# Kernel optimization log

Measured on AMD Instinct MI355X. Metric: run time of the kernel, lower is better.

Reference implementation:

```python
import jax, jax.numpy as jnp
import numpy as np

B, F, E, A = 8192, 50, 16, 16

def setup_inputs() -> dict:
    key = jax.random.key(0)
    ks = jax.random.split(key, 9)
    feat_index = jax.random.randint(ks[0], (B, F), 0, F, dtype=jnp.int64)
    feat_value = jax.random.uniform(ks[1], (B, F), dtype=jnp.float32)
    emb_table = jax.random.uniform(ks[2], (F, E), minval=-0.05, maxval=0.05, dtype=jnp.float32)
    attention_w = 0.05 * jax.random.normal(ks[3], (E, A), dtype=jnp.float32)
    attention_b = 0.05 * jax.random.normal(ks[4], (A,), dtype=jnp.float32)
    attention_h = 0.05 * jax.random.normal(ks[5], (A,), dtype=jnp.float32)
    attention_p = jnp.ones((E, 1), dtype=jnp.float32)
    lin_w = 0.05 * jax.random.normal(ks[6], (F, 1), dtype=jnp.float32)
    lin_b = jnp.zeros((1,), dtype=jnp.float32)
    return {"feat_index": feat_index, "feat_value": feat_value, "emb_table": emb_table,
            "attention_w": attention_w, "attention_b": attention_b, "attention_h": attention_h,
            "attention_p": attention_p, "lin_w": lin_w, "lin_b": lin_b}

def reference(feat_index, feat_value, emb_table, attention_w, attention_b, attention_h, attention_p, lin_w, lin_b):
    # embedding lookup + value scaling: [B, F, E]
    emb = emb_table[feat_index] * feat_value[:, :, None]
    # all pairwise (i<j) elementwise products: [B, P, E], P = F*(F-1)/2
    ii, jj = np.triu_indices(emb.shape[1], k=1)
    ewp = emb[:, ii, :] * emb[:, jj, :]
    # attention MLP: relu(ewp @ W + b) . h  -> unnormalized exp scores
    wx = jnp.einsum('bpe,ea->bpa', ewp, attention_w) + attention_b
    score = jnp.exp(jnp.sum(jax.nn.relu(wx) * attention_h, axis=2))  # [B, P]
    att = score / jnp.sum(score, axis=1, keepdims=True)
    # attention-weighted pooling over interactions, then project to scalar
    pooled = jnp.einsum('bp,bpe->be', att, ewp)  # [B, E]
    y_deep = pooled @ attention_p  # [B, 1]
    # linear part: Dense(1, relu) over field axis of emb^T [B, E, F], then sum over E
    y_lin = jnp.sum(jax.nn.relu(jnp.einsum('bfe,fo->beo', emb, lin_w) + lin_b), axis=1)  # [B, 1]
    return y_deep + y_lin
```

## Files before the change

kernel.cpp:

```cpp
#include <hip/hip_runtime.h>
#include <math.h>

#define FDIM  50
#define EDIM  16
#define ADIM  16
#define NPAIR 1225
#define BROWS 32
#define NTHREADS 1024
#define NWAVE 16
#define NPAD  (NPAIR + 2 * NWAVE)
#define FBLK  1024

typedef _Float16 half8v __attribute__((ext_vector_type(8)));
typedef __fp16   h16x8  __attribute__((ext_vector_type(8)));
typedef __fp16   h16x2  __attribute__((ext_vector_type(2)));
typedef float    f32x16 __attribute__((ext_vector_type(16)));

__device__ inline f32x16 mfma32x32x16f16(half8v a, half8v b, f32x16 c) {
    return __builtin_amdgcn_mfma_f32_32x32x16_f16(
        __builtin_bit_cast(h16x8, a), __builtin_bit_cast(h16x8, b), c, 0, 0, 0);
}

__global__ __launch_bounds__(NTHREADS) void afm_fwd(
    const int*   __restrict__ feat_index,
    const float* __restrict__ feat_value,
    const float* __restrict__ emb_table,
    const float* __restrict__ attn_w,
    const float* __restrict__ attn_b,
    const float* __restrict__ attn_h,
    const float* __restrict__ attn_p,
    const float* __restrict__ lin_w,
    const float* __restrict__ lin_b,
    float*       __restrict__ out)
{
    __shared__ __align__(16) _Float16 embLds[FDIM * 512];
    __shared__ unsigned ijLds[NPAD];
    __shared__ float    redLds[NWAVE][BROWS][2];
    __shared__ float    ylinLds[BROWS];
    __shared__ float    lwLds[FDIM];

    const int t    = threadIdx.x;
    const int lane = t & 63;
    const int wv   = t >> 6;
    const int hi   = lane >> 5;
    const int col  = lane & 31;
    const int b0   = blockIdx.x * BROWS;

    if (t < FDIM) lwLds[t] = lin_w[t];

    for (int p = t; p < NPAD; p += NTHREADS) {
        int pc = (p < NPAIR) ? p : NPAIR - 1;
        float tq = 9801.0f - 8.0f * (float)pc;
        int ii = (int)((99.0f - sqrtf(tq)) * 0.5f);
        ii = max(0, min(48, ii));
        while (ii < 48 && (49*(ii+1) - (((ii+1)*ii)>>1)) <= pc) ++ii;
        while (ii > 0  && (49*ii - ((ii*(ii-1))>>1)) > pc) --ii;
        int q  = 49*ii - ((ii*(ii-1))>>1);
        int jj = ii + 1 + (pc - q);
        ijLds[p] = ((unsigned)(ii*FBLK) << 16) | (unsigned)(jj*FBLK);
    }

    for (int f = t >> 6; f < FDIM; f += NWAVE) {
        int   fi = feat_index[(b0 + col) * FDIM + f];
        float fv = feat_value[(b0 + col) * FDIM + f];
        const float4* tr = (const float4*)(emb_table + (size_t)fi * EDIM + hi * 8);
        float4 v0 = tr[0], v1 = tr[1];
        half8v hh;
        hh[0] = (_Float16)(v0.x * fv); hh[1] = (_Float16)(v0.y * fv);
        hh[2] = (_Float16)(v0.z * fv); hh[3] = (_Float16)(v0.w * fv);
        hh[4] = (_Float16)(v1.x * fv); hh[5] = (_Float16)(v1.y * fv);
        hh[6] = (_Float16)(v1.z * fv); hh[7] = (_Float16)(v1.w * fv);
        *(half8v*)&embLds[f * 512 + lane * 8] = hh;
    }
    __syncthreads();

    if (t < 512) {
        int bb = t >> 4, e = t & 15;
        int off = (e >> 3) * 256 + bb * 8 + (e & 7);
        float acc = lin_b[0];
        #pragma unroll
        for (int f = 0; f < FDIM; ++f)
            acc = fmaf((float)embLds[f * 512 + off], lwLds[f], acc);
        acc = fmaxf(acc, 0.0f);
        acc += __shfl_xor(acc, 1);
        acc += __shfl_xor(acc, 2);
        acc += __shfl_xor(acc, 4);
        acc += __shfl_xor(acc, 8);
        if (e == 0) ylinLds[bb] = acc;
    }

    half8v fragA1;
    #pragma unroll
    for (int e = 0; e < 8; ++e) {
        int k = hi * 8 + e;
        float av = (col < ADIM) ? attn_w[k * ADIM + col]
                 : (col == ADIM) ? attn_p[k] : 0.0f;
        fragA1[e] = (_Float16)av;
    }
    half8v fragA2;
    f32x16 biasC;
    #pragma unroll
    for (int e = 0; e < 8; ++e) {
        int r = (e & 3) + 8 * (e >> 2) + 4 * hi;
        fragA2[e]  = (_Float16)(attn_h[r] * 1.44269504f);
        biasC[e]   = attn_b[r];
        biasC[e+8] = 0.f;
    }
    f32x16 zeroC;
    #pragma unroll
    for (int r = 0; r < 16; ++r) zeroC[r] = 0.f;

    const char* ebase = (const char*)embLds;
    const unsigned laddr = (unsigned)lane * 16u;

    float num = 0.f, den = 0.f;
    unsigned u0   = ijLds[wv];
    half8v   ei   = *(const half8v*)(ebase + (u0 >> 16)     + laddr);
    half8v   ej   = *(const half8v*)(ebase + (u0 & 0xffffu) + laddr);
    unsigned unxt = ijLds[wv + NWAVE];

    #pragma unroll 2
    for (int p = wv; p < NPAIR; p += NWAVE) {
        half8v ei_n = *(const half8v*)(ebase + (unxt >> 16)     + laddr);
        half8v ej_n = *(const half8v*)(ebase + (unxt & 0xffffu) + laddr);
        unsigned u2 = ijLds[p + 2 * NWAVE];

        half8v prod = ei * ej;
        f32x16 acc1 = mfma32x32x16f16(fragA1, prod, biasC);

        h16x2 q01 = __builtin_amdgcn_cvt_pkrtz(acc1[0], acc1[1]);
        h16x2 q23 = __builtin_amdgcn_cvt_pkrtz(acc1[2], acc1[3]);
        h16x2 q45 = __builtin_amdgcn_cvt_pkrtz(acc1[4], acc1[5]);
        h16x2 q67 = __builtin_amdgcn_cvt_pkrtz(acc1[6], acc1[7]);
        h16x8 pk = __builtin_shufflevector(
                       __builtin_shufflevector(q01, q23, 0, 1, 2, 3),
                       __builtin_shufflevector(q45, q67, 0, 1, 2, 3),
                       0, 1, 2, 3, 4, 5, 6, 7);
        half8v rf = __builtin_bit_cast(half8v, pk);
        half8v zf;
        #pragma unroll
        for (int e = 0; e < 8; ++e) zf[e] = (_Float16)0;
#if __has_builtin(__builtin_elementwise_max)
        rf = __builtin_elementwise_max(rf, zf);
#else
        #pragma unroll
        for (int e = 0; e < 8; ++e) rf[e] = rf[e] > (_Float16)0 ? rf[e] : (_Float16)0;
#endif
        f32x16 acc2 = mfma32x32x16f16(fragA2, rf, zeroC);

        float sc = __builtin_amdgcn_exp2f(acc2[0]);
        if (hi) den += sc;
        else    num = fmaf(sc, acc1[8], num);

        ei = ei_n; ej = ej_n; unxt = u2;
    }

    if (hi) redLds[wv][col][1] = den;
    else    redLds[wv][col][0] = num;
    __syncthreads();

    if (t < BROWS) {
        float nn = 0.f, dd = 0.f;
        #pragma unroll
        for (int w = 0; w < NWAVE; ++w) { nn += redLds[w][t][0]; dd += redLds[w][t][1]; }
        out[b0 + t] = nn / dd + ylinLds[t];
    }
}

extern "C" void kernel_launch(void* const* d_in, const int* in_sizes, int n_in,
                              void* d_out, int out_size, void* d_ws, size_t ws_size,
                              hipStream_t stream) {
    const int*   feat_index = (const int*)  d_in[0];
    const float* feat_value = (const float*)d_in[1];
    const float* emb_table  = (const float*)d_in[2];
    const float* attn_w     = (const float*)d_in[3];
    const float* attn_b     = (const float*)d_in[4];
    const float* attn_h     = (const float*)d_in[5];
    const float* attn_p     = (const float*)d_in[6];
    const float* lin_w      = (const float*)d_in[7];
    const float* lin_b      = (const float*)d_in[8];
    float* outp = (float*)d_out;

    dim3 grid(out_size / BROWS);
    dim3 block(NTHREADS);
    afm_fwd<<<grid, block, 0, stream>>>(feat_index, feat_value, emb_table,
                                        attn_w, attn_b, attn_h, attn_p,
                                        lin_w, lin_b, outp);
}
```

Measured before the change: 29.83 us.

## Give each wave a contiguous pair chunk and iterate i/j directly

Removes the precomputed pair-index table in LDS. Each wave now takes a contiguous chunk of 77 pairs, finds its starting (i,j) once, and walks j inside nested loops while keeping e_i in registers. This cuts the index loads and the e_i reload per pair. In exchange it adds an inner loop with a variable trip count, which may hurt unrolling, and a prefetch that reads one row past the end (the reason for the padded LDS buffer).

```diff
diff --git a/kernel.cpp b/kernel.cpp
--- a/kernel.cpp
+++ b/kernel.cpp
@@ -8,7 +8,7 @@
 #define BROWS 32
 #define NTHREADS 1024
 #define NWAVE 16
-#define NPAD  (NPAIR + 2 * NWAVE)
+#define CHUNK 77
 #define FBLK  1024
 
 typedef _Float16 half8v __attribute__((ext_vector_type(8)));
@@ -33,11 +33,10 @@
     const float* __restrict__ lin_b,
     float*       __restrict__ out)
 {
-    __shared__ __align__(16) _Float16 embLds[FDIM * 512];
-    __shared__ unsigned ijLds[NPAD];
-    __shared__ float    redLds[NWAVE][BROWS][2];
-    __shared__ float    ylinLds[BROWS];
-    __shared__ float    lwLds[FDIM];
+    __shared__ __align__(16) _Float16 embLds[(FDIM + 1) * 512];
+    __shared__ float redLds[NWAVE][BROWS][2];
+    __shared__ float ylinLds[BROWS];
+    __shared__ float lwLds[FDIM];
 
     const int t    = threadIdx.x;
     const int lane = t & 63;
@@ -47,18 +46,6 @@
     const int b0   = blockIdx.x * BROWS;
 
     if (t < FDIM) lwLds[t] = lin_w[t];
-
-    for (int p = t; p < NPAD; p += NTHREADS) {
-        int pc = (p < NPAIR) ? p : NPAIR - 1;
-        float tq = 9801.0f - 8.0f * (float)pc;
-        int ii = (int)((99.0f - sqrtf(tq)) * 0.5f);
-        ii = max(0, min(48, ii));
-        while (ii < 48 && (49*(ii+1) - (((ii+1)*ii)>>1)) <= pc) ++ii;
-        while (ii > 0  && (49*ii - ((ii*(ii-1))>>1)) > pc) --ii;
-        int q  = 49*ii - ((ii*(ii-1))>>1);
-        int jj = ii + 1 + (pc - q);
-        ijLds[p] = ((unsigned)(ii*FBLK) << 16) | (unsigned)(jj*FBLK);
-    }
 
     for (int f = t >> 6; f < FDIM; f += NWAVE) {
         int   fi = feat_index[(b0 + col) * FDIM + f];
@@ -113,46 +100,59 @@
     const char* ebase = (const char*)embLds;
     const unsigned laddr = (unsigned)lane * 16u;
 
+    const int pbeg = wv * CHUNK;
+    const int pend = (pbeg + CHUNK < NPAIR) ? pbeg + CHUNK : NPAIR;
+
+    float tq = 9801.0f - 8.0f * (float)pbeg;
+    int i = (int)((99.0f - sqrtf(tq)) * 0.5f);
+    i = max(0, min(48, i));
+    while (i < 48 && (49*(i+1) - (((i+1)*i)>>1)) <= pbeg) ++i;
+    while (i > 0  && (49*i - ((i*(i-1))>>1)) > pbeg) --i;
+    int j = i + 1 + (pbeg - (49*i - ((i*(i-1))>>1)));
+
     float num = 0.f, den = 0.f;
-    unsigned u0   = ijLds[wv];
-    half8v   ei   = *(const half8v*)(ebase + (u0 >> 16)     + laddr);
-    half8v   ej   = *(const half8v*)(ebase + (u0 & 0xffffu) + laddr);
-    unsigned unxt = ijLds[wv + NWAVE];
+    int p = pbeg;
+    while (p < pend) {
+        int len = FDIM - j;
+        if (len > pend - p) len = pend - p;
+        half8v ei = *(const half8v*)(ebase + (unsigned)(i * FBLK) + laddr);
+        unsigned aj = (unsigned)(j * FBLK) + laddr;
+        half8v ejn = *(const half8v*)(ebase + aj);
+        for (int n = 0; n < len; ++n) {
+            half8v ej = ejn;
+            aj += FBLK;
+            ejn = *(const half8v*)(ebase + aj);
 
-    #pragma unroll 2
-    for (int p = wv; p < NPAIR; p += NWAVE) {
-        half8v ei_n = *(const half8v*)(ebase + (unxt >> 16)     + laddr);
-        half8v ej_n = *(const half8v*)(ebase + (unxt & 0xffffu) + laddr);
-        unsigned u2 = ijLds[p + 2 * NWAVE];
+            half8v prod = ei * ej;
+            f32x16 acc1 = mfma32x32x16f16(fragA1, prod, biasC);
 
-        half8v prod = ei * ej;
-        f32x16 acc1 = mfma32x32x16f16(fragA1, prod, biasC);
+            h16x2 q01 = __builtin_amdgcn_cvt_pkrtz(acc1[0], acc1[1]);
+            h16x2 q23 = __builtin_amdgcn_cvt_pkrtz(acc1[2], acc1[3]);
+            h16x2 q45 = __builtin_amdgcn_cvt_pkrtz(acc1[4], acc1[5]);
+            h16x2 q67 = __builtin_amdgcn_cvt_pkrtz(acc1[6], acc1[7]);
+            h16x8 pk = __builtin_shufflevector(
+                           __builtin_shufflevector(q01, q23, 0, 1, 2, 3),
+                           __builtin_shufflevector(q45, q67, 0, 1, 2, 3),
+                           0, 1, 2, 3, 4, 5, 6, 7);
+            half8v rf = __builtin_bit_cast(half8v, pk);
+            half8v zf;
+            #pragma unroll
+            for (int e = 0; e < 8; ++e) zf[e] = (_Float16)0;
+#if __has_builtin(__builtin_elementwise_max)
+            rf = __builtin_elementwise_max(rf, zf);
+#else
+            #pragma unroll
+            for (int e = 0; e < 8; ++e) rf[e] = rf[e] > (_Float16)0 ? rf[e] : (_Float16)0;
+#endif
+            f32x16 acc2 = mfma32x32x16f16(fragA2, rf, zeroC);
 
-        h16x2 q01 = __builtin_amdgcn_cvt_pkrtz(acc1[0], acc1[1]);
-        h16x2 q23 = __builtin_amdgcn_cvt_pkrtz(acc1[2], acc1[3]);
-        h16x2 q45 = __builtin_amdgcn_cvt_pkrtz(acc1[4], acc1[5]);
-        h16x2 q67 = __builtin_amdgcn_cvt_pkrtz(acc1[6], acc1[7]);
-        h16x8 pk = __builtin_shufflevector(
-                       __builtin_shufflevector(q01, q23, 0, 1, 2, 3),
-                       __builtin_shufflevector(q45, q67, 0, 1, 2, 3),
-                       0, 1, 2, 3, 4, 5, 6, 7);
-        half8v rf = __builtin_bit_cast(half8v, pk);
-        half8v zf;
-        #pragma unroll
-        for (int e = 0; e < 8; ++e) zf[e] = (_Float16)0;
-#if __has_builtin(__builtin_elementwise_max)
-        rf = __builtin_elementwise_max(rf, zf);
-#else
-        #pragma unroll
-        for (int e = 0; e < 8; ++e) rf[e] = rf[e] > (_Float16)0 ? rf[e] : (_Float16)0;
-#endif
-        f32x16 acc2 = mfma32x32x16f16(fragA2, rf, zeroC);
-
-        float sc = __builtin_amdgcn_exp2f(acc2[0]);
-        if (hi) den += sc;
-        else    num = fmaf(sc, acc1[8], num);
-
-        ei = ei_n; ej = ej_n; unxt = u2;
+            float sc = __builtin_amdgcn_exp2f(acc2[0]);
+            if (hi) den += sc;
+            else    num = fmaf(sc, acc1[8], num);
+        }
+        p += len;
+        ++i;
+        j = i + 1;
     }
 
     if (hi) redLds[wv][col][1] = den;
```

Result: faster. 28.94 us (-3.0%).

## Process two independent pairs per wave iteration with 12 waves and bias-folded exp correction

Applied to the files above, without the earlier changes.

Drops the block from 16 to 12 waves. Each wave now handles two independent pair chains per loop iteration over a fixed trip count, with a single tail pair given to wave 0, so the two MFMA/exp chains can interleave. The second MFMA reuses biasC as its accumulator input instead of zero, and a per-lane exp2 correction factor cancels that offset so the branchy num/den update becomes unconditional. The risks are fewer waves in flight, extra register pressure, and subtle correctness depending on how the bias offset lines up with the accumulator element that is read.

```diff
diff --git a/kernel.cpp b/kernel.cpp
--- a/kernel.cpp
+++ b/kernel.cpp
@@ -6,9 +6,11 @@
 #define ADIM  16
 #define NPAIR 1225
 #define BROWS 32
-#define NTHREADS 1024
-#define NWAVE 16
-#define NPAD  (NPAIR + 2 * NWAVE)
+#define NTHREADS 768
+#define NWAVE 12
+#define NST   24
+#define KITER 51
+#define NPAD  1248
 #define FBLK  1024
 
 typedef _Float16 half8v __attribute__((ext_vector_type(8)));
@@ -35,9 +37,9 @@
 {
     __shared__ __align__(16) _Float16 embLds[FDIM * 512];
     __shared__ unsigned ijLds[NPAD];
-    __shared__ float    redLds[NWAVE][BROWS][2];
-    __shared__ float    ylinLds[BROWS];
-    __shared__ float    lwLds[FDIM];
+    __shared__ float redLds[NWAVE][BROWS][2];
+    __shared__ float ylinLds[BROWS];
+    __shared__ float lwLds[FDIM];
 
     const int t    = threadIdx.x;
     const int lane = t & 63;
@@ -106,28 +108,74 @@
         biasC[e]   = attn_b[r];
         biasC[e+8] = 0.f;
     }
-    f32x16 zeroC;
-    #pragma unroll
-    for (int r = 0; r < 16; ++r) zeroC[r] = 0.f;
+    const float corr = __builtin_amdgcn_exp2f(-attn_b[4 * hi]);
 
     const char* ebase = (const char*)embLds;
     const unsigned laddr = (unsigned)lane * 16u;
 
-    float num = 0.f, den = 0.f;
-    unsigned u0   = ijLds[wv];
-    half8v   ei   = *(const half8v*)(ebase + (u0 >> 16)     + laddr);
-    half8v   ej   = *(const half8v*)(ebase + (u0 & 0xffffu) + laddr);
-    unsigned unxt = ijLds[wv + NWAVE];
-
-    #pragma unroll 2
-    for (int p = wv; p < NPAIR; p += NWAVE) {
-        half8v ei_n = *(const half8v*)(ebase + (unxt >> 16)     + laddr);
-        half8v ej_n = *(const half8v*)(ebase + (unxt & 0xffffu) + laddr);
-        unsigned u2 = ijLds[p + 2 * NWAVE];
-
-        half8v prod = ei * ej;
+    const int s0 = wv * 2;
+    unsigned uA = ijLds[s0];
+    unsigned uB = ijLds[s0 + 1];
+    float numA = 0.f, denA = 0.f, numB = 0.f, denB = 0.f;
+
+    for (int k = 0; k < KITER; ++k) {
+        half8v eiA = *(const half8v*)(ebase + (uA >> 16)     + laddr);
+        half8v ejA = *(const half8v*)(ebase + (uA & 0xffffu) + laddr);
+        half8v eiB = *(const half8v*)(ebase + (uB >> 16)     + laddr);
+        half8v ejB = *(const half8v*)(ebase + (uB & 0xffffu) + laddr);
+        int nidx = s0 + NST * (k + 1);
+        uA = ijLds[nidx];
+        uB = ijLds[nidx + 1];
+
+        {
+            half8v prod = eiA * ejA;
+            f32x16 acc1 = mfma32x32x16f16(fragA1, prod, biasC);
+            h16x2 q01 = __builtin_amdgcn_cvt_pkrtz(acc1[0], acc1[1]);
+            h16x2 q23 = __builtin_amdgcn_cvt_pkrtz(acc1[2], acc1[3]);
+            h16x2 q45 = __builtin_amdgcn_cvt_pkrtz(acc1[4], acc1[5]);
+            h16x2 q67 = __builtin_amdgcn_cvt_pkrtz(acc1[6], acc1[7]);
+            h16x8 pk = __builtin_shufflevector(
+                           __builtin_shufflevector(q01, q23, 0, 1, 2, 3),
+                           __builtin_shufflevector(q45, q67, 0, 1, 2, 3),
+                           0, 1, 2, 3, 4, 5, 6, 7);
+            half8v rf = __builtin_bit_cast(half8v, pk);
+            half8v zf;
+            #pragma unroll
+            for (int e = 0; e < 8; ++e) zf[e] = (_Float16)0;
+            rf = __builtin_elementwise_max(rf, zf);
+            f32x16 acc2 = mfma32x32x16f16(fragA2, rf, biasC);
+            float sc = __builtin_amdgcn_exp2f(acc2[0]);
+            denA += sc;
+            numA = fmaf(sc, acc1[8], numA);
+        }
+        {
+            half8v prod = eiB * ejB;
+            f32x16 acc1 = mfma32x32x16f16(fragA1, prod, biasC);
+            h16x2 q01 = __builtin_amdgcn_cvt_pkrtz(acc1[0], acc1[1]);
+            h16x2 q23 = __builtin_amdgcn_cvt_pkrtz(acc1[2], acc1[3]);
+            h16x2 q45 = __builtin_amdgcn_cvt_pkrtz(acc1[4], acc1[5]);
+            h16x2 q67 = __builtin_amdgcn_cvt_pkrtz(acc1[6], acc1[7]);
+            h16x8 pk = __builtin_shufflevector(
+                           __builtin_shufflevector(q01, q23, 0, 1, 2, 3),
+                           __builtin_shufflevector(q45, q67, 0, 1, 2, 3),
+                           0, 1, 2, 3, 4, 5, 6, 7);
+            half8v rf = __builtin_bit_cast(half8v, pk);
+            half8v zf;
+            #pragma unroll
+            for (int e = 0; e < 8; ++e) zf[e] = (_Float16)0;
+            rf = __builtin_elementwise_max(rf, zf);
+            f32x16 acc2 = mfma32x32x16f16(fragA2, rf, biasC);
+            float sc = __builtin_amdgcn_exp2f(acc2[0]);
+            denB += sc;
+            numB = fmaf(sc, acc1[8], numB);
+        }
+    }
+
+    if (wv == 0) {
+        half8v eiA = *(const half8v*)(ebase + (uA >> 16)     + laddr);
+        half8v ejA = *(const half8v*)(ebase + (uA & 0xffffu) + laddr);
+        half8v prod = eiA * ejA;
         f32x16 acc1 = mfma32x32x16f16(fragA1, prod, biasC);
-
         h16x2 q01 = __builtin_amdgcn_cvt_pkrtz(acc1[0], acc1[1]);
         h16x2 q23 = __builtin_amdgcn_cvt_pkrtz(acc1[2], acc1[3]);
         h16x2 q45 = __builtin_amdgcn_cvt_pkrtz(acc1[4], acc1[5]);
@@ -140,21 +188,15 @@
         half8v zf;
         #pragma unroll
         for (int e = 0; e < 8; ++e) zf[e] = (_Float16)0;
-#if __has_builtin(__builtin_elementwise_max)
         rf = __builtin_elementwise_max(rf, zf);
-#else
-        #pragma unroll
-        for (int e = 0; e < 8; ++e) rf[e] = rf[e] > (_Float16)0 ? rf[e] : (_Float16)0;
-#endif
-        f32x16 acc2 = mfma32x32x16f16(fragA2, rf, zeroC);
-
+        f32x16 acc2 = mfma32x32x16f16(fragA2, rf, biasC);
         float sc = __builtin_amdgcn_exp2f(acc2[0]);
-        if (hi) den += sc;
-        else    num = fmaf(sc, acc1[8], num);
-
-        ei = ei_n; ej = ej_n; unxt = u2;
-    }
-
+        denA += sc;
+        numA = fmaf(sc, acc1[8], numA);
+    }
+
+    float num = (numA + numB) * corr;
+    float den = (denA + denB) * corr;
     if (hi) redLds[wv][col][1] = den;
     else    redLds[wv][col][0] = num;
     __syncthreads();
```

New measurement: 29.27 us. No clear change (-1.9%).
